# Kernel optimization log

Measured on AMD Instinct MI355X. Metric: run time of the kernel, lower is better.

## Reference

```python
import jax, jax.numpy as jnp
import numpy as np

B, N, C_IN = 4, 120000, 4
FEAT, H, W = 128, 128, 128
PC_RANGE = (-50.0, -50.0, -5.0, 50.0, 50.0, 3.0)
EPS = 1e-5  # BatchNorm eps (torch default)


def setup_inputs() -> dict:
    key = jax.random.key(0)
    ks = jax.random.split(key, 16)
    # LiDAR-like point cloud: x,y spread ~[-90,90] (mostly in-range), z ~[-6,6], intensity ~N(0,1)
    points = jax.random.normal(ks[0], (B, N, C_IN), jnp.float32) * jnp.array([30.0, 30.0, 2.0, 1.0], jnp.float32)

    def lin(k, o, i):
        return jax.random.normal(k, (o, i), jnp.float32) * (1.0 / np.sqrt(i))

    def bn(k, c):
        k1, k2, k3, k4 = jax.random.split(k, 4)
        return (jax.random.normal(k1, (c,), jnp.float32) * 0.1 + 1.0,  # gamma
                jax.random.normal(k2, (c,), jnp.float32) * 0.1,        # beta
                jax.random.normal(k3, (c,), jnp.float32) * 0.1,        # running mean
                jax.random.uniform(k4, (c,), jnp.float32, 0.5, 1.5))   # running var

    g1, be1, m1, v1 = bn(ks[3], 64)
    g2, be2, m2, v2 = bn(ks[4], 128)
    g3, be3, m3, v3 = bn(ks[5], FEAT)
    return {
        'points': points,
        'W1': lin(ks[6], 64, C_IN), 'b1': jax.random.normal(ks[7], (64,), jnp.float32) * 0.01,
        'g1': g1, 'be1': be1, 'm1': m1, 'v1': v1,
        'W2': lin(ks[8], 128, 64), 'b2': jax.random.normal(ks[9], (128,), jnp.float32) * 0.01,
        'g2': g2, 'be2': be2, 'm2': m2, 'v2': v2,
        'W3': lin(ks[10], FEAT, 128), 'b3': jax.random.normal(ks[11], (FEAT,), jnp.float32) * 0.01,
        'g3': g3, 'be3': be3, 'm3': m3, 'v3': v3,
    }


def _bn_relu(x, g, b, m, v):
    # eval-mode BatchNorm1d + ReLU, applied over last (channel) axis
    return jax.nn.relu((x - m) * jax.lax.rsqrt(v + EPS) * g + b)


def _forward(points, W1, b1, g1, be1, m1, v1, W2, b2, g2, be2, m2, v2, W3, b3, g3, be3, m3, v3):
    # Per-point MLP (1x1 convs == per-point linears): [B,N,4] -> [B,N,FEAT]
    h = _bn_relu(jnp.einsum('bni,oi->bno', points, W1) + b1, g1, be1, m1, v1)
    h = _bn_relu(jnp.einsum('bni,oi->bno', h, W2) + b2, g2, be2, m2, v2)
    feats = _bn_relu(jnp.einsum('bni,oi->bno', h, W3) + b3, g3, be3, m3, v3)  # [B,N,FEAT]

    x, y = points[..., 0], points[..., 1]
    x_norm = (x - PC_RANGE[0]) / (PC_RANGE[3] - PC_RANGE[0])
    y_norm = (y - PC_RANGE[1]) / (PC_RANGE[4] - PC_RANGE[1])
    valid = (x_norm >= 0) & (x_norm <= 1) & (y_norm >= 0) & (y_norm <= 1)  # [B,N]

    gx = jnp.clip((x_norm * (W - 1)).astype(jnp.int32), 0, W - 1)
    gy = jnp.clip((y_norm * (H - 1)).astype(jnp.int32), 0, H - 1)
    bidx = jnp.arange(B, dtype=jnp.int32)[:, None]
    # invalid points routed to a dummy segment B*H*W
    seg = jnp.where(valid, bidx * (H * W) + gy * W + gx, B * H * W)  # [B,N]

    bev = jax.ops.segment_max(feats.reshape(B * N, FEAT), seg.reshape(B * N),
                              num_segments=B * H * W + 1)  # [B*H*W+1, FEAT]
    bev = bev[:B * H * W]
    bev = jnp.where(jnp.isneginf(bev), jnp.zeros((), bev.dtype), bev)  # empty cells stay 0
    return bev.reshape(B, H, W, FEAT).transpose(0, 3, 1, 2)  # [B, FEAT, H, W]


def reference(points, W1, b1, g1, be1, m1, v1, W2, b2, g2, be2, m2, v2, W3, b3, g3, be3, m3, v3):
    return _forward(points, W1, b1, g1, be1, m1, v1, W2, b2, g2, be2, m2, v2, W3, b3, g3, be3, m3, v3)
```

## Files before the change

### kernel.cpp

```cpp
#include <hip/hip_runtime.h>
#include <hip/hip_fp16.h>

#define BB 4
#define NN 120000
#define FEAT 128
#define HH 128
#define WW 128
#define NPTS (BB*NN)
#define HW (HH*WW)

#define OW1    0
#define OB1    256
#define OW2P   320
#define OB2    4416
#define OW3P   4544
#define OB3    12736
#define OW3F   12864
#define OW2F   21056
#define OCNT   25152
#define OOFF   90688
#define ONV    156224
#define OCELLS 156288
#define OSIDX  636288
#define OSCELL 1116288
#define OFEATS 1596288
#define OBEV   1596288
#define BEV_ELEMS (BB*HW*FEAT)

#if defined(__has_builtin)
#if __has_builtin(__builtin_amdgcn_fdot2)
#define HAS_FDOT2 1
#endif
#endif

typedef _Float16 hv2 __attribute__((ext_vector_type(2)));
typedef _Float16 f16x8 __attribute__((ext_vector_type(8)));
typedef float    f32x4 __attribute__((ext_vector_type(4)));
typedef float    fv16  __attribute__((ext_vector_type(16)));

__device__ __forceinline__ unsigned pk2(float a, float b) {
    __half2 h = __floats2half2_rn(a, b);
    return __builtin_bit_cast(unsigned, h);
}

__device__ __forceinline__ float dot2(unsigned a, unsigned b, float c) {
#ifdef HAS_FDOT2
    return __builtin_amdgcn_fdot2(__builtin_bit_cast(hv2, a),
                                  __builtin_bit_cast(hv2, b), c, false);
#else
    __half2 ah = __builtin_bit_cast(__half2, a), bh = __builtin_bit_cast(__half2, b);
    c = fmaf(__low2float(ah), __low2float(bh), c);
    return fmaf(__high2float(ah), __high2float(bh), c);
#endif
}

__device__ __forceinline__ unsigned hmax2u(unsigned a, unsigned b) {
    unsigned al = a & 0xFFFFu, bl = b & 0xFFFFu;
    unsigned ah = a & 0xFFFF0000u, bh = b & 0xFFFF0000u;
    unsigned lo = (al > bl) ? al : bl;
    unsigned hi = (ah > bh) ? ah : bh;
    return lo | hi;
}

__device__ __forceinline__ unsigned h16(float v) {
    _Float16 h = (_Float16)v;
    return (unsigned)__builtin_bit_cast(unsigned short, h);
}

__global__ void fold_weights_k(
    const float* __restrict__ W1, const float* __restrict__ b1,
    const float* __restrict__ g1, const float* __restrict__ be1,
    const float* __restrict__ m1, const float* __restrict__ v1,
    const float* __restrict__ W2, const float* __restrict__ b2,
    const float* __restrict__ g2, const float* __restrict__ be2,
    const float* __restrict__ m2, const float* __restrict__ v2,
    const float* __restrict__ W3, const float* __restrict__ b3,
    const float* __restrict__ g3, const float* __restrict__ be3,
    const float* __restrict__ m3, const float* __restrict__ v3,
    float* __restrict__ wf)
{
    unsigned* wu = (unsigned*)wf;
    int idx = blockIdx.x * 256 + threadIdx.x;
    const float EPSV = 1e-5f;
    if (idx < 256) {
        int o = idx >> 2;
        float s = g1[o] * rsqrtf(v1[o] + EPSV);
        wf[OW1 + idx] = W1[idx] * s;
    } else if (idx < 320) {
        int o = idx - 256;
        float s = g1[o] * rsqrtf(v1[o] + EPSV);
        wf[idx] = (b1[o] - m1[o]) * s + be1[o];
    } else if (idx < 4416) {
        int j = idx - OW2P;
        int r = j >> 7, o = j & 127;
        float s = g2[o] * rsqrtf(v2[o] + EPSV);
        wu[idx] = pk2(W2[o * 64 + 2 * r] * s, W2[o * 64 + 2 * r + 1] * s);
    } else if (idx < 4544) {
        int o = idx - OB2;
        float s = g2[o] * rsqrtf(v2[o] + EPSV);
        wf[idx] = (b2[o] - m2[o]) * s + be2[o];
    } else if (idx < 12736) {
        int j = idx - OW3P;
        int ch = j >> 9, rem = j & 511;
        int r = rem >> 3, jj = rem & 7;
        int o = ch * 8 + jj;
        float s = g3[o] * rsqrtf(v3[o] + EPSV);
        wu[idx] = pk2(W3[o * 128 + 2 * r] * s, W3[o * 128 + 2 * r + 1] * s);
    } else if (idx < 12864) {
        int o = idx - OB3;
        float s = g3[o] * rsqrtf(v3[o] + EPSV);
        wf[idx] = (b3[o] - m3[o]) * s + be3[o];
    } else if (idx < 21056) {
        int u = idx - OW3F;
        int tile = u >> 8, w = u & 255;
        int l = w >> 2, q = w & 3;
        int n = (tile >> 2) * 16 + (l & 15);
        int k = (tile & 3) * 32 + ((l >> 4) << 3) + 2 * q;
        float s = g3[n] * rsqrtf(v3[n] + EPSV);
        wu[idx] = pk2(W3[n * 128 + k] * s, W3[n * 128 + k + 1] * s);
    } else if (idx < 25152) {
        int u = idx - OW2F;
        int tile = u >> 8, w = u & 255;
        int l = w >> 2, q = w & 3;
        int n = (tile >> 1) * 16 + (l & 15);
        int k = (tile & 1) * 32 + ((l >> 4) << 3) + 2 * q;
        float s = g2[n] * rsqrtf(v2[n] + EPSV);
        wu[idx] = pk2(W2[n * 64 + k] * s, W2[n * 64 + k + 1] * s);
    } else if (idx < 25152 + 65536) {
        ((int*)wf)[OCNT + idx - 25152] = 0;
    }
}

__global__ __launch_bounds__(256)
void cells_hist_k(const float4* __restrict__ pts, int* __restrict__ cells,
                  int* __restrict__ cnt)
{
    int tid = blockIdx.x * 256 + threadIdx.x;
    float4 p = pts[tid];
    float xn = (p.x - (-50.0f)) / (50.0f - (-50.0f));
    float yn = (p.y - (-50.0f)) / (50.0f - (-50.0f));
    bool valid = (xn >= 0.0f) && (xn <= 1.0f) && (yn >= 0.0f) && (yn <= 1.0f);
    int gx = min(max((int)(xn * 127.0f), 0), 127);
    int gy = min(max((int)(yn * 127.0f), 0), 127);
    int b = tid / NN;
    int cell = valid ? (b * HW + gy * WW + gx) : -1;
    cells[tid] = cell;
    if (valid) atomicAdd(&cnt[cell], 1);
}

__global__ __launch_bounds__(1024)
void scan_k(const int* __restrict__ cnt, int* __restrict__ off, int* __restrict__ nvp)
{
    __shared__ int wsum[16];
    int t = threadIdx.x;
    int lane = t & 63, w = t >> 6;
    int base = t * 64;
    int s = 0;
#pragma unroll 8
    for (int j = 0; j < 64; ++j) s += cnt[base + j];
    int v = s;
#pragma unroll
    for (int d = 1; d < 64; d <<= 1) {
        int u = __shfl_up(v, d);
        if (lane >= d) v += u;
    }
    if (lane == 63) wsum[w] = v;
    __syncthreads();
    if (t == 0) {
        int r = 0;
#pragma unroll
        for (int k = 0; k < 16; ++k) { int x = wsum[k]; wsum[k] = r; r += x; }
        nvp[0] = r;
    }
    __syncthreads();
    int excl = (v - s) + wsum[w];
    int r = excl;
#pragma unroll 8
    for (int j = 0; j < 64; ++j) { off[base + j] = r; r += cnt[base + j]; }
}

__global__ __launch_bounds__(256)
void scatter_idx_k(const int* __restrict__ cells, int* __restrict__ off,
                   int* __restrict__ sidx, int* __restrict__ scell)
{
    int tid = blockIdx.x * 256 + threadIdx.x;
    int c = cells[tid];
    if (c >= 0) {
        int pos = atomicAdd(&off[c], 1);
        sidx[pos] = tid;
        scell[pos] = c;
    }
}

__global__ __launch_bounds__(256)
void fused_mlp_k(const float4* __restrict__ pts, const float* __restrict__ wf,
                 const int* __restrict__ sidx, const int* __restrict__ nvp,
                 uint4* __restrict__ feats4)
{
    __shared__ __align__(16) _Float16 h2t[4][16 * 132];
    const unsigned* wu = (const unsigned*)wf;
    const uint4* bf2 = (const uint4*)(wu + OW2F);
    const uint4* bf3 = (const uint4*)(wu + OW3F);
    const int tid = threadIdx.x, wv = tid >> 6, l = tid & 63;
    const int nv = nvp[0];
    const int M0 = (blockIdx.x * 4 + wv) * 16;
    if (M0 >= nv) return;
    const int l15 = l & 15, q = l >> 4;
    const int par = l15 & 1;

    const int slot = M0 + l15;
    const int pidx = (slot < nv) ? sidx[slot] : 0;
    float4 p = pts[pidx];

    uint4 a2[2];
#pragma unroll
    for (int kt = 0; kt < 2; ++kt) {
        unsigned w4[4];
#pragma unroll
        for (int t = 0; t < 4; ++t) {
            int f = kt * 32 + q * 8 + 2 * t;
            const float* wa = wf + OW1 + f * 4;
            float a = wf[OB1 + f], b = wf[OB1 + f + 1];
            a = fmaf(wa[0], p.x, a); a = fmaf(wa[1], p.y, a);
            a = fmaf(wa[2], p.z, a); a = fmaf(wa[3], p.w, a);
            b = fmaf(wa[4], p.x, b); b = fmaf(wa[5], p.y, b);
            b = fmaf(wa[6], p.z, b); b = fmaf(wa[7], p.w, b);
            w4[t] = pk2(fmaxf(a, 0.f), fmaxf(b, 0.f));
        }
        uint4 v; v.x = w4[0]; v.y = w4[1]; v.z = w4[2]; v.w = w4[3];
        a2[kt] = v;
    }

    unsigned* myh2 = (unsigned*)&h2t[wv][0];

#pragma unroll
    for (int nt = 0; nt < 8; ++nt) {
        f32x4 acc = {0.f, 0.f, 0.f, 0.f};
        acc = __builtin_amdgcn_mfma_f32_16x16x32_f16(
            __builtin_bit_cast(f16x8, a2[0]),
            __builtin_bit_cast(f16x8, bf2[(nt * 2 + 0) * 64 + l]), acc, 0, 0, 0);
        acc = __builtin_amdgcn_mfma_f32_16x16x32_f16(
            __builtin_bit_cast(f16x8, a2[1]),
            __builtin_bit_cast(f16x8, bf2[(nt * 2 + 1) * 64 + l]), acc, 0, 0, 0);
        float bias = wf[OB2 + nt * 16 + l15];
        unsigned wrd[4];
#pragma unroll
        for (int rr = 0; rr < 4; ++rr) {
            unsigned h = h16(fmaxf(acc[rr] + bias, 0.f));
            unsigned nb = (unsigned)__builtin_amdgcn_update_dpp(
                0, (int)h, 0xB1 , 0xF, 0xF, false);
            wrd[rr] = par ? ((nb & 0xFFFFu) | (h << 16)) : (h | (nb << 16));
        }
        unsigned* base = myh2 + nt * 8 + (l15 >> 1);
#pragma unroll
        for (int i = 0; i < 2; ++i) {
            int rr = 2 * par + i;
            base[(q * 4 + rr) * 66] = wrd[rr];
        }
    }

    uint4 a3[4];
#pragma unroll
    for (int kt = 0; kt < 4; ++kt)
        a3[kt] = *(const uint4*)&h2t[wv][l15 * 132 + kt * 32 + q * 8];

#pragma unroll 2
    for (int nt = 0; nt < 8; ++nt) {
        f32x4 acc = {0.f, 0.f, 0.f, 0.f};
#pragma unroll
        for (int kt = 0; kt < 4; ++kt)
            acc = __builtin_amdgcn_mfma_f32_16x16x32_f16(
                __builtin_bit_cast(f16x8, a3[kt]),
                __builtin_bit_cast(f16x8, bf3[(nt * 4 + kt) * 64 + l]), acc, 0, 0, 0);
        float bias = wf[OB3 + nt * 16 + l15];
        unsigned wrd[4];
#pragma unroll
        for (int rr = 0; rr < 4; ++rr) {
            unsigned h = h16(fmaxf(acc[rr] + bias, 0.f));
            unsigned nb = (unsigned)__builtin_amdgcn_update_dpp(
                0, (int)h, 0xB1, 0xF, 0xF, false);
            wrd[rr] = par ? ((nb & 0xFFFFu) | (h << 16)) : (h | (nb << 16));
        }
        unsigned* base = myh2 + nt * 8 + (l15 >> 1);
#pragma unroll
        for (int i = 0; i < 2; ++i) {
            int rr = 2 * par + i;
            base[(q * 4 + rr) * 66] = wrd[rr];
        }
    }

    const int pt = l >> 2, part = l & 3;
#pragma unroll
    for (int i = 0; i < 4; ++i) {
        uint4 vv = *(const uint4*)&h2t[wv][pt * 132 + (part * 4 + i) * 8];
        feats4[(size_t)(M0 + pt) * 16 + part * 4 + i] = vv;
    }
}

__global__ __launch_bounds__(256)
void reduce_k(const unsigned* __restrict__ feats, const int* __restrict__ off,
              const int* __restrict__ cnt, float* __restrict__ out)
{
    __shared__ float tile[128][65];
    const int tid = threadIdx.x;
    const int w = tid >> 6, l = tid & 63;
    const int l15 = l & 15, lq = l >> 4;
    const int c0 = blockIdx.x * 64;
    const uint4* f4 = (const uint4*)feats;

#pragma unroll 2
    for (int cc = 0; cc < 16; ++cc) {
        int c = c0 + w * 16 + cc;
        int n = cnt[c];
        int start = off[c] - n;
        uint4 m = {0u, 0u, 0u, 0u};
        const uint4* fp = f4 + (size_t)(start + lq) * 16 + l15;
#pragma unroll 1
        for (int p = 0; p < n; p += 4) {
            if (p + lq < n) {
                uint4 v = fp[(size_t)p * 16];
                m.x = hmax2u(m.x, v.x); m.y = hmax2u(m.y, v.y);
                m.z = hmax2u(m.z, v.z); m.w = hmax2u(m.w, v.w);
            }
        }
#pragma unroll
        for (int d = 16; d <= 32; d <<= 1) {
            m.x = hmax2u(m.x, (unsigned)__shfl_xor((int)m.x, d));
            m.y = hmax2u(m.y, (unsigned)__shfl_xor((int)m.y, d));
            m.z = hmax2u(m.z, (unsigned)__shfl_xor((int)m.z, d));
            m.w = hmax2u(m.w, (unsigned)__shfl_xor((int)m.w, d));
        }
        if (lq == 0) {
            int f0 = 8 * l15, cl = w * 16 + cc;
            __half2 hx = __builtin_bit_cast(__half2, m.x);
            __half2 hy = __builtin_bit_cast(__half2, m.y);
            __half2 hz = __builtin_bit_cast(__half2, m.z);
            __half2 hw = __builtin_bit_cast(__half2, m.w);
            tile[f0 + 0][cl] = __low2float(hx); tile[f0 + 1][cl] = __high2float(hx);
            tile[f0 + 2][cl] = __low2float(hy); tile[f0 + 3][cl] = __high2float(hy);
            tile[f0 + 4][cl] = __low2float(hz); tile[f0 + 5][cl] = __high2float(hz);
            tile[f0 + 6][cl] = __low2float(hw); tile[f0 + 7][cl] = __high2float(hw);
        }
    }
    __syncthreads();
    const int b = c0 >> 14;
    const int cxy = c0 & (HW - 1);
#pragma unroll 4
    for (int k = 0; k < 32; ++k) {
        int idx = k * 256 + tid;
        int f = idx >> 6, cl = idx & 63;
        out[((size_t)(b * 128 + f)) * HW + cxy + cl] = tile[f][cl];
    }
}

#define DPPMAX(A, D, S) { \
    float _pv = __int_as_float(__builtin_amdgcn_update_dpp( \
        0, __float_as_int(A), 0x110 | (D), 0xF, 0xF, false)); \
    A = (S) ? fmaxf(A, _pv) : A; }

__global__ __launch_bounds__(256)
void mlp_atomic_k(const float4* __restrict__ pts, const float* __restrict__ wf,
                  const int* __restrict__ sidx, const int* __restrict__ scell,
                  const int* __restrict__ nvp, float* __restrict__ bev, int layout)
{
    __shared__ unsigned h1s[32 * 256];
    __shared__ unsigned h2s[64 * 256];
    const unsigned* wu = (const unsigned*)wf;
    const int tid = threadIdx.x;
    const int slot = blockIdx.x * 256 + tid;
    const int nv = nvp[0];
    if ((slot & ~63) >= nv) return;
    const int lane = tid & 63;
    const int l15 = lane & 15;
    const bool live = slot < nv;
    const int cell = live ? scell[slot] : -1;
    const int pidx = live ? sidx[slot] : 0;
    float4 p = pts[pidx];

    int c1 = __shfl_up(cell, 1), c2 = __shfl_up(cell, 2);
    int c4 = __shfl_up(cell, 4), c8 = __shfl_up(cell, 8);
    bool s1 = (l15 >= 1) && (c1 == cell);
    bool s2 = (l15 >= 2) && (c2 == cell);
    bool s4 = (l15 >= 4) && (c4 == cell);
    bool s8 = (l15 >= 8) && (c8 == cell);
    int cn = __shfl_down(cell, 1);
    bool tail = (l15 == 15) || (cn != cell);

#pragma unroll
    for (int i = 0; i < 32; ++i) {
        const float* wa = wf + OW1 + 8 * i;
        float a = wf[OB1 + 2 * i], b = wf[OB1 + 2 * i + 1];
        a = fmaf(wa[0], p.x, a); a = fmaf(wa[1], p.y, a);
        a = fmaf(wa[2], p.z, a); a = fmaf(wa[3], p.w, a);
        b = fmaf(wa[4], p.x, b); b = fmaf(wa[5], p.y, b);
        b = fmaf(wa[6], p.z, b); b = fmaf(wa[7], p.w, b);
        h1s[i * 256 + tid] = pk2(fmaxf(a, 0.0f), fmaxf(b, 0.0f));
    }
#pragma unroll 1
    for (int o0 = 0; o0 < 128; o0 += 16) {
        fv16 acc;
#pragma unroll
        for (int j = 0; j < 16; ++j) acc[j] = wf[OB2 + o0 + j];
#pragma unroll
        for (int r = 0; r < 32; ++r) {
            unsigned h1r = h1s[r * 256 + tid];
            const unsigned* wr = wu + OW2P + r * 128 + o0;
#pragma unroll
            for (int j = 0; j < 16; ++j) acc[j] = dot2(h1r, wr[j], acc[j]);
        }
#pragma unroll
        for (int j = 0; j < 16; j += 2)
            h2s[((o0 + j) >> 1) * 256 + tid] =
                pk2(fmaxf(acc[j], 0.f), fmaxf(acc[j + 1], 0.f));
    }

    int* ob = (int*)bev;
    long base0;
    if (layout == 0) base0 = (long)cell * 128;
    else             base0 = (long)(cell >> 14) * (128 * HW) + (cell & (HW - 1));

#pragma unroll 1
    for (int ch = 0; ch < 16; ++ch) {
        float a0=wf[OB3+ch*8+0], a1=wf[OB3+ch*8+1], a2=wf[OB3+ch*8+2], a3=wf[OB3+ch*8+3];
        float a4=wf[OB3+ch*8+4], a5=wf[OB3+ch*8+5], a6=wf[OB3+ch*8+6], a7=wf[OB3+ch*8+7];
        const unsigned* wq = wu + OW3P + ch * 512;
#pragma unroll
        for (int r = 0; r < 64; ++r) {
            unsigned h2r = h2s[r * 256 + tid];
            a0 = dot2(h2r, wq[r*8+0], a0); a1 = dot2(h2r, wq[r*8+1], a1);
            a2 = dot2(h2r, wq[r*8+2], a2); a3 = dot2(h2r, wq[r*8+3], a3);
            a4 = dot2(h2r, wq[r*8+4], a4); a5 = dot2(h2r, wq[r*8+5], a5);
            a6 = dot2(h2r, wq[r*8+6], a6); a7 = dot2(h2r, wq[r*8+7], a7);
        }
        float av[8] = {a0,a1,a2,a3,a4,a5,a6,a7};
#pragma unroll
        for (int j = 0; j < 8; ++j) {
            float aj = fmaxf(av[j], 0.0f);
            DPPMAX(aj, 1, s1); DPPMAX(aj, 2, s2);
            DPPMAX(aj, 4, s4); DPPMAX(aj, 8, s8);
            av[j] = aj;
        }
        if (tail && cell >= 0) {
            if (layout == 0) {
#pragma unroll
                for (int j = 0; j < 8; ++j)
                    atomicMax(ob + base0 + ch * 8 + j, __float_as_int(av[j]));
            } else {
#pragma unroll
                for (int j = 0; j < 8; ++j)
                    atomicMax(ob + base0 + (long)(ch * 8 + j) * HW, __float_as_int(av[j]));
            }
        }
    }
}

__global__ void transpose_bev_k(const float* __restrict__ bev, float* __restrict__ out)
{
    __shared__ float tile[32][129];
    const int tid = threadIdx.x;
    const int cell0 = blockIdx.x * 32;
#pragma unroll
    for (int k = 0; k < 16; ++k) {
        int idx = k * 256 + tid;
        int c = idx >> 7, f = idx & 127;
        tile[c][f] = bev[(size_t)(cell0 + c) * 128 + f];
    }
    __syncthreads();
    const int b = cell0 >> 14;
    const int cl0 = cell0 & (HW - 1);
#pragma unroll
    for (int k = 0; k < 16; ++k) {
        int idx = k * 256 + tid;
        int f = idx >> 5, c = idx & 31;
        out[(size_t)(b * 128 + f) * HW + cl0 + c] = tile[c][f];
    }
}

extern "C" void kernel_launch(void* const* d_in, const int* in_sizes, int n_in,
                              void* d_out, int out_size, void* d_ws, size_t ws_size,
                              hipStream_t stream)
{
    const float* points = (const float*)d_in[0];
    const float* W1 = (const float*)d_in[1];  const float* b1 = (const float*)d_in[2];
    const float* g1 = (const float*)d_in[3];  const float* be1 = (const float*)d_in[4];
    const float* m1 = (const float*)d_in[5];  const float* v1 = (const float*)d_in[6];
    const float* W2 = (const float*)d_in[7];  const float* b2 = (const float*)d_in[8];
    const float* g2 = (const float*)d_in[9];  const float* be2 = (const float*)d_in[10];
    const float* m2 = (const float*)d_in[11]; const float* v2 = (const float*)d_in[12];
    const float* W3 = (const float*)d_in[13]; const float* b3 = (const float*)d_in[14];
    const float* g3 = (const float*)d_in[15]; const float* be3 = (const float*)d_in[16];
    const float* m3 = (const float*)d_in[17]; const float* v3 = (const float*)d_in[18];

    float* wsf = (float*)d_ws;
    int*   wsi = (int*)d_ws;
    const size_t need_full = ((size_t)OFEATS + (size_t)NPTS * 64) * 4;
    const size_t need_bev  = ((size_t)OBEV + BEV_ELEMS) * 4;

    fold_weights_k<<<(25152 + 65536 + 255) / 256, 256, 0, stream>>>(
        W1, b1, g1, be1, m1, v1, W2, b2, g2, be2, m2, v2, W3, b3, g3, be3, m3, v3, wsf);

    cells_hist_k<<<NPTS / 256, 256, 0, stream>>>(
        (const float4*)points, wsi + OCELLS, wsi + OCNT);
    scan_k<<<1, 1024, 0, stream>>>(wsi + OCNT, wsi + OOFF, wsi + ONV);
    scatter_idx_k<<<NPTS / 256, 256, 0, stream>>>(
        wsi + OCELLS, wsi + OOFF, wsi + OSIDX, wsi + OSCELL);

    if (ws_size >= need_full) {
        uint4* feats4 = (uint4*)(wsi + OFEATS);
        fused_mlp_k<<<NPTS / 64, 256, 0, stream>>>(
            (const float4*)points, wsf, wsi + OSIDX, wsi + ONV, feats4);
        reduce_k<<<BB * HW / 64, 256, 0, stream>>>(
            (const unsigned*)feats4, wsi + OOFF, wsi + OCNT, (float*)d_out);
    } else if (ws_size >= need_bev) {
        float* bev = wsf + OBEV;
        (void)hipMemsetAsync(bev, 0, (size_t)BEV_ELEMS * sizeof(float), stream);
        mlp_atomic_k<<<NPTS / 256, 256, 0, stream>>>(
            (const float4*)points, wsf, wsi + OSIDX, wsi + OSCELL, wsi + ONV, bev, 0);
        transpose_bev_k<<<HW * BB / 32, 256, 0, stream>>>(bev, (float*)d_out);
    } else {
        (void)hipMemsetAsync(d_out, 0, (size_t)out_size * sizeof(float), stream);
        mlp_atomic_k<<<NPTS / 256, 256, 0, stream>>>(
            (const float4*)points, wsf, wsi + OSIDX, wsi + OSCELL, wsi + ONV,
            (float*)d_out, 1);
    }
}
```

Before: 277.4 us.

## Compute MLP transposed so layer outputs stay in registers, dropping LDS staging

After: 287.9 us. 1.04x slower.

```diff
diff --git a/kernel.cpp b/kernel.cpp
--- a/kernel.cpp
+++ b/kernel.cpp
@@ -17,23 +17,29 @@
 #define OB3    12736
 #define OW3F   12864
 #define OW2F   21056
-#define OCNT   25152
-#define OOFF   90688
-#define ONV    156224
-#define OCELLS 156288
-#define OSIDX  636288
-#define OSCELL 1116288
-#define OFEATS 1596288
-#define OBEV   1596288
+#define OB2L   25152
+#define OB3L   27200
+#define OCNT   29248
+#define OOFF   94784
+#define ONV    160320
+#define OCELLS 160384
+#define OSIDX  640384
+#define OSCELL 1120384
+#define OFEATS 1600384
+#define OBEV   1600384
 #define BEV_ELEMS (BB*HW*FEAT)
 
 #if defined(__has_builtin)
 #if __has_builtin(__builtin_amdgcn_fdot2)
 #define HAS_FDOT2 1
 #endif
+#if __has_builtin(__builtin_amdgcn_cvt_pkrtz)
+#define HAS_PKRTZ 1
 #endif
+#endif
 
 typedef _Float16 hv2 __attribute__((ext_vector_type(2)));
+typedef __fp16   pkv2 __attribute__((ext_vector_type(2)));
 typedef _Float16 f16x8 __attribute__((ext_vector_type(8)));
 typedef float    f32x4 __attribute__((ext_vector_type(4)));
 typedef float    fv16  __attribute__((ext_vector_type(16)));
@@ -41,6 +47,15 @@
 __device__ __forceinline__ unsigned pk2(float a, float b) {
     __half2 h = __floats2half2_rn(a, b);
     return __builtin_bit_cast(unsigned, h);
+}
+
+__device__ __forceinline__ unsigned pkz(float a, float b) {
+#ifdef HAS_PKRTZ
+    pkv2 h = __builtin_amdgcn_cvt_pkrtz(a, b);
+    return __builtin_bit_cast(unsigned, h);
+#else
+    return pk2(a, b);
+#endif
 }
 
 __device__ __forceinline__ float dot2(unsigned a, unsigned b, float c) {
@@ -62,9 +77,9 @@
     return lo | hi;
 }
 
-__device__ __forceinline__ unsigned h16(float v) {
-    _Float16 h = (_Float16)v;
-    return (unsigned)__builtin_bit_cast(unsigned short, h);
+__device__ __forceinline__ f32x4 mfma16(uint4 a, uint4 b, f32x4 c) {
+    return __builtin_amdgcn_mfma_f32_16x16x32_f16(
+        __builtin_bit_cast(f16x8, a), __builtin_bit_cast(f16x8, b), c, 0, 0, 0);
 }
 
 __global__ void fold_weights_k(
@@ -113,11 +128,15 @@
     } else if (idx < 21056) {
         int u = idx - OW3F;
         int tile = u >> 8, w = u & 255;
-        int l = w >> 2, q = w & 3;
-        int n = (tile >> 2) * 16 + (l & 15);
-        int k = (tile & 3) * 32 + ((l >> 4) << 3) + 2 * q;
-        float s = g3[n] * rsqrtf(v3[n] + EPSV);
-        wu[idx] = pk2(W3[n * 128 + k] * s, W3[n * 128 + k + 1] * s);
+        int l = w >> 2, qq = w & 3;
+        int q = l >> 4;
+        int m3 = (tile >> 2) * 16 + (l & 15);
+        int kt = tile & 3;
+        int j0 = 2 * qq, j1 = 2 * qq + 1;
+        int f0 = ((j0 >> 2) * 4 + kt) * 16 + q * 4 + (j0 & 3);
+        int f1 = ((j1 >> 2) * 4 + kt) * 16 + q * 4 + (j1 & 3);
+        float s = g3[m3] * rsqrtf(v3[m3] + EPSV);
+        wu[idx] = pk2(W3[m3 * 128 + f0] * s, W3[m3 * 128 + f1] * s);
     } else if (idx < 25152) {
         int u = idx - OW2F;
         int tile = u >> 8, w = u & 255;
@@ -126,8 +145,20 @@
         int k = (tile & 1) * 32 + ((l >> 4) << 3) + 2 * q;
         float s = g2[n] * rsqrtf(v2[n] + EPSV);
         wu[idx] = pk2(W2[n * 64 + k] * s, W2[n * 64 + k + 1] * s);
-    } else if (idx < 25152 + 65536) {
-        ((int*)wf)[OCNT + idx - 25152] = 0;
+    } else if (idx < 27200) {
+        int f = idx - OB2L;
+        int mt = f >> 8, l = (f >> 2) & 63, rr = f & 3;
+        int o = mt * 16 + (l >> 4) * 4 + rr;
+        float s = g2[o] * rsqrtf(v2[o] + EPSV);
+        wf[idx] = (b2[o] - m2[o]) * s + be2[o];
+    } else if (idx < 29248) {
+        int f = idx - OB3L;
+        int mt = f >> 8, l = (f >> 2) & 63, rr = f & 3;
+        int o = mt * 16 + (l >> 4) * 4 + rr;
+        float s = g3[o] * rsqrtf(v3[o] + EPSV);
+        wf[idx] = (b3[o] - m3[o]) * s + be3[o];
+    } else if (idx < 29248 + 65536) {
+        ((int*)wf)[OCNT + idx - 29248] = 0;
     }
 }
 
@@ -195,18 +226,18 @@
 __global__ __launch_bounds__(256)
 void fused_mlp_k(const float4* __restrict__ pts, const float* __restrict__ wf,
                  const int* __restrict__ sidx, const int* __restrict__ nvp,
-                 uint4* __restrict__ feats4)
-{
-    __shared__ __align__(16) _Float16 h2t[4][16 * 132];
+                 uint2* __restrict__ feats2)
+{
     const unsigned* wu = (const unsigned*)wf;
-    const uint4* bf2 = (const uint4*)(wu + OW2F);
-    const uint4* bf3 = (const uint4*)(wu + OW3F);
+    const uint4* A2 = (const uint4*)(wu + OW2F);
+    const uint4* A3 = (const uint4*)(wu + OW3F);
+    const float4* B2L = (const float4*)(wf + OB2L);
+    const float4* B3L = (const float4*)(wf + OB3L);
     const int tid = threadIdx.x, wv = tid >> 6, l = tid & 63;
     const int nv = nvp[0];
     const int M0 = (blockIdx.x * 4 + wv) * 16;
     if (M0 >= nv) return;
     const int l15 = l & 15, q = l >> 4;
-    const int par = l15 & 1;
 
     const int slot = M0 + l15;
     const int pidx = (slot < nv) ? sidx[slot] : 0;
@@ -225,75 +256,43 @@
             a = fmaf(wa[2], p.z, a); a = fmaf(wa[3], p.w, a);
             b = fmaf(wa[4], p.x, b); b = fmaf(wa[5], p.y, b);
             b = fmaf(wa[6], p.z, b); b = fmaf(wa[7], p.w, b);
-            w4[t] = pk2(fmaxf(a, 0.f), fmaxf(b, 0.f));
+            w4[t] = pkz(fmaxf(a, 0.f), fmaxf(b, 0.f));
         }
         uint4 v; v.x = w4[0]; v.y = w4[1]; v.z = w4[2]; v.w = w4[3];
         a2[kt] = v;
     }
 
-    unsigned* myh2 = (unsigned*)&h2t[wv][0];
-
-#pragma unroll
-    for (int nt = 0; nt < 8; ++nt) {
-        f32x4 acc = {0.f, 0.f, 0.f, 0.f};
-        acc = __builtin_amdgcn_mfma_f32_16x16x32_f16(
-            __builtin_bit_cast(f16x8, a2[0]),
-            __builtin_bit_cast(f16x8, bf2[(nt * 2 + 0) * 64 + l]), acc, 0, 0, 0);
-        acc = __builtin_amdgcn_mfma_f32_16x16x32_f16(
-            __builtin_bit_cast(f16x8, a2[1]),
-            __builtin_bit_cast(f16x8, bf2[(nt * 2 + 1) * 64 + l]), acc, 0, 0, 0);
-        float bias = wf[OB2 + nt * 16 + l15];
-        unsigned wrd[4];
-#pragma unroll
-        for (int rr = 0; rr < 4; ++rr) {
-            unsigned h = h16(fmaxf(acc[rr] + bias, 0.f));
-            unsigned nb = (unsigned)__builtin_amdgcn_update_dpp(
-                0, (int)h, 0xB1 , 0xF, 0xF, false);
-            wrd[rr] = par ? ((nb & 0xFFFFu) | (h << 16)) : (h | (nb << 16));
-        }
-        unsigned* base = myh2 + nt * 8 + (l15 >> 1);
-#pragma unroll
-        for (int i = 0; i < 2; ++i) {
-            int rr = 2 * par + i;
-            base[(q * 4 + rr) * 66] = wrd[rr];
-        }
-    }
-
-    uint4 a3[4];
-#pragma unroll
-    for (int kt = 0; kt < 4; ++kt)
-        a3[kt] = *(const uint4*)&h2t[wv][l15 * 132 + kt * 32 + q * 8];
-
-#pragma unroll 2
-    for (int nt = 0; nt < 8; ++nt) {
-        f32x4 acc = {0.f, 0.f, 0.f, 0.f};
+    unsigned pk[8][2];
+#pragma unroll
+    for (int mt = 0; mt < 8; ++mt) {
+        float4 bv = B2L[mt * 64 + l];
+        f32x4 acc = {bv.x, bv.y, bv.z, bv.w};
+        acc = mfma16(A2[(mt * 2 + 0) * 64 + l], a2[0], acc);
+        acc = mfma16(A2[(mt * 2 + 1) * 64 + l], a2[1], acc);
+        pk[mt][0] = pkz(fmaxf(acc[0], 0.f), fmaxf(acc[1], 0.f));
+        pk[mt][1] = pkz(fmaxf(acc[2], 0.f), fmaxf(acc[3], 0.f));
+    }
+
+    uint4 b3[4];
+#pragma unroll
+    for (int kt = 0; kt < 4; ++kt) {
+        uint4 v;
+        v.x = pk[kt][0];     v.y = pk[kt][1];
+        v.z = pk[kt + 4][0]; v.w = pk[kt + 4][1];
+        b3[kt] = v;
+    }
+
+#pragma unroll
+    for (int mt = 0; mt < 8; ++mt) {
+        float4 bv = B3L[mt * 64 + l];
+        f32x4 acc = {bv.x, bv.y, bv.z, bv.w};
 #pragma unroll
         for (int kt = 0; kt < 4; ++kt)
-            acc = __builtin_amdgcn_mfma_f32_16x16x32_f16(
-                __builtin_bit_cast(f16x8, a3[kt]),
-                __builtin_bit_cast(f16x8, bf3[(nt * 4 + kt) * 64 + l]), acc, 0, 0, 0);
-        float bias = wf[OB3 + nt * 16 + l15];
-        unsigned wrd[4];
-#pragma unroll
-        for (int rr = 0; rr < 4; ++rr) {
-            unsigned h = h16(fmaxf(acc[rr] + bias, 0.f));
-            unsigned nb = (unsigned)__builtin_amdgcn_update_dpp(
-                0, (int)h, 0xB1, 0xF, 0xF, false);
-            wrd[rr] = par ? ((nb & 0xFFFFu) | (h << 16)) : (h | (nb << 16));
-        }
-        unsigned* base = myh2 + nt * 8 + (l15 >> 1);
-#pragma unroll
-        for (int i = 0; i < 2; ++i) {
-            int rr = 2 * par + i;
-            base[(q * 4 + rr) * 66] = wrd[rr];
-        }
-    }
-
-    const int pt = l >> 2, part = l & 3;
-#pragma unroll
-    for (int i = 0; i < 4; ++i) {
-        uint4 vv = *(const uint4*)&h2t[wv][pt * 132 + (part * 4 + i) * 8];
-        feats4[(size_t)(M0 + pt) * 16 + part * 4 + i] = vv;
+            acc = mfma16(A3[(mt * 4 + kt) * 64 + l], b3[kt], acc);
+        uint2 o;
+        o.x = pkz(fmaxf(acc[0], 0.f), fmaxf(acc[1], 0.f));
+        o.y = pkz(fmaxf(acc[2], 0.f), fmaxf(acc[3], 0.f));
+        feats2[(size_t)slot * 32 + mt * 4 + q] = o;
     }
 }
 
@@ -496,7 +495,7 @@
     const size_t need_full = ((size_t)OFEATS + (size_t)NPTS * 64) * 4;
     const size_t need_bev  = ((size_t)OBEV + BEV_ELEMS) * 4;
 
-    fold_weights_k<<<(25152 + 65536 + 255) / 256, 256, 0, stream>>>(
+    fold_weights_k<<<(29248 + 65536 + 255) / 256, 256, 0, stream>>>(
         W1, b1, g1, be1, m1, v1, W2, b2, g2, be2, m2, v2, W3, b3, g3, be3, m3, v3, wsf);
 
     cells_hist_k<<<NPTS / 256, 256, 0, stream>>>(
@@ -506,11 +505,11 @@
         wsi + OCELLS, wsi + OOFF, wsi + OSIDX, wsi + OSCELL);
 
     if (ws_size >= need_full) {
-        uint4* feats4 = (uint4*)(wsi + OFEATS);
         fused_mlp_k<<<NPTS / 64, 256, 0, stream>>>(
-            (const float4*)points, wsf, wsi + OSIDX, wsi + ONV, feats4);
+            (const float4*)points, wsf, wsi + OSIDX, wsi + ONV,
+            (uint2*)(wsi + OFEATS));
         reduce_k<<<BB * HW / 64, 256, 0, stream>>>(
-            (const unsigned*)feats4, wsi + OOFF, wsi + OCNT, (float*)d_out);
+            (const unsigned*)(wsi + OFEATS), wsi + OOFF, wsi + OCNT, (float*)d_out);
     } else if (ws_size >= need_bev) {
         float* bev = wsf + OBEV;
         (void)hipMemsetAsync(bev, 0, (size_t)BEV_ELEMS * sizeof(float), stream);
```
